# Kernel optimization log

Measured on AMD Instinct MI355X. Metric: run time of the kernel, lower is better.

## Reference

```python
import jax, jax.numpy as jnp
import numpy as np

EPS = 1e-05
FACT = 2.0
REJECT_RATIO = 1.0


def setup_inputs() -> dict:
    key = jax.random.key(0)
    k1, k2 = jax.random.split(key)
    B, N = 8, 4096
    pc1 = jax.random.normal(k1, (B, 4, N), dtype=jnp.float32)
    pc2 = jax.random.normal(k2, (B, 4, N), dtype=jnp.float32)
    # homogeneous coordinates: last row = 1
    pc1 = pc1.at[:, 3, :].set(1.0)
    pc2 = pc2.at[:, 3, :].set(1.0)
    return {"pc1": pc1, "pc2": pc2}


def _rot_to_quat(R):
    # standard rotation-matrix -> quaternion (w, x, y, z)
    r00, r11, r22 = R[0, 0], R[1, 1], R[2, 2]
    qw = 0.5 * jnp.sqrt(jnp.maximum(1e-12, 1.0 + r00 + r11 + r22))
    qx = 0.5 * jnp.sqrt(jnp.maximum(0.0, 1.0 + r00 - r11 - r22))
    qy = 0.5 * jnp.sqrt(jnp.maximum(0.0, 1.0 - r00 + r11 - r22))
    qz = 0.5 * jnp.sqrt(jnp.maximum(0.0, 1.0 - r00 - r11 + r22))
    qx = jnp.where(R[2, 1] - R[1, 2] < 0, -qx, qx)
    qy = jnp.where(R[0, 2] - R[2, 0] < 0, -qy, qy)
    qz = jnp.where(R[1, 0] - R[0, 1] < 0, -qz, qz)
    return jnp.stack([qw, qx, qy, qz])


def _normalize_rotmat(R):
    # operates on COLUMNS, like the torch code (R[:, 2] etc.)
    z = R[:, 2] / jnp.linalg.norm(R[:, 2])
    y = R[:, 1]
    x = jnp.cross(y, z)
    x = x / jnp.linalg.norm(x)
    y = jnp.cross(z, x)
    return jnp.stack([x, y, z], axis=1)


def _norm_tf(pc):
    # T = diag(1/std) @ [I | -mean]  (std is unbiased, as torch.std)
    std = jnp.std(pc[:3, :], axis=1, ddof=1)
    mean = jnp.mean(pc[:3, :], axis=1)
    T = jnp.zeros((4, 4), dtype=pc.dtype)
    T = T.at[jnp.arange(3), jnp.arange(3)].set(1.0 / std)
    T = T.at[:3, 3].set(-mean / std)
    T = T.at[3, 3].set(1.0)
    return T


def _per_sample(pc1, pc2):
    # ---- soft_knn: pairwise squared distance over xyz ----
    p1, p2 = pc1[:3], pc2[:3]  # (3, N)
    d = ((p1 ** 2).sum(0)[:, None]
         - 2.0 * jnp.einsum('dn,dm->nm', p1, p2)
         + (p2 ** 2).sum(0)[None, :])            # (N1, N2)
    W = jax.nn.softmax(FACT / jnp.clip(d, EPS, None), axis=1)
    pc_nearest = pc2 @ W.T                        # (4, N1) soft-gathered points

    # ---- soft_outlier_rejection ----
    dist = jnp.linalg.norm(pc1 - pc_nearest, axis=0)
    filt = jax.nn.sigmoid((dist - dist.mean() * REJECT_RATIO - EPS) * -1e10)

    # ---- dlt(pc1, pc_nearest, filt) ----
    T2 = _norm_tf(pc_nearest)
    pc2n = T2 @ pc_nearest
    T1 = _norm_tf(pc1)
    pc1n = T1 @ pc1

    mask = (filt > 0.5).astype(pc1.dtype)         # hard inlier mask (sigmoid slope 1e10)
    N = pc1.shape[1]
    a = pc1n.T                                    # (N, 4)
    z4 = jnp.zeros((N, 4), dtype=pc1.dtype)
    row0 = jnp.concatenate([z4, -pc2n[2][:, None] * a, pc2n[1][:, None] * a], axis=1)
    row1 = jnp.concatenate([pc2n[2][:, None] * a, z4, -pc2n[0][:, None] * a], axis=1)
    M = (jnp.stack([row0, row1], axis=1) * mask[:, None, None]).reshape(2 * N, 12)

    _, _, Vh = jnp.linalg.svd(M, full_matrices=False)
    p = Vh[-1]                                    # null-space vector (12,)
    p = jnp.where(p[10] < 0, -p, p)
    p = p / jnp.sqrt(p[8] ** 2 + p[9] ** 2 + p[10] ** 2)

    T = jnp.zeros((4, 4), dtype=pc1.dtype)
    T = T.at[:3, :].set(p.reshape(3, 4)).at[3, 3].set(1.0)
    T = jnp.linalg.inv(T2) @ T @ T1
    R = _normalize_rotmat(T[:3, :3])
    T = T.at[:3, :3].set(R)
    return T, _rot_to_quat(R), T[:3, 3]


def reference(pc1, pc2):
    T, q, t = jax.vmap(_per_sample)(pc1, pc2)
    return T, q, t
```

## Files before the change

kernel.cpp:

```cpp
#include <hip/hip_runtime.h>
#include <math.h>

#define NPTS 4096
#define EPSC 1e-5f
#define F2C (2.0f*1.44269504088896340736f)

#if __has_builtin(__builtin_amdgcn_exp2f)
#define FEXP2 __builtin_amdgcn_exp2f
#else
#define FEXP2(x) __expf((x)*0.6931471805599453f)
#endif

#define IDX(i,j) ((i)*((i)+1)/2 + (j))

__global__ void __launch_bounds__(256) k_soft(const float* __restrict__ pc1,
                                              const float* __restrict__ pc2,
                                              float4* __restrict__ part4,
                                              float* __restrict__ partZ){
  constexpr int CHN = 256, NC = 16;
  int bid = blockIdx.x;
  int chunk = bid & (NC-1), rb = (bid/NC) & 15, b = bid/(NC*16);

  __shared__ float4 sp[CHN];
  {
    const float* p2 = pc2 + (size_t)b*4*NPTS + chunk*CHN;
    for (int m = threadIdx.x; m < CHN; m += 256){
      float x = p2[m], y = p2[m+NPTS], z = p2[m+2*NPTS];
      sp[m] = make_float4(x, y, z, x*x + y*y + z*z);
    }
  }
  __syncthreads();

  int n = rb*256 + threadIdx.x;
  const float* p1 = pc1 + (size_t)b*4*NPTS + n;
  float x1 = p1[0], y1 = p1[NPTS], z1 = p1[2*NPTS];
  float q1 = x1*x1 + y1*y1 + z1*z1;
  float mx = -2.f*x1, my = -2.f*y1, mz = -2.f*z1;

  float4 c0 = sp[0];
  float d0 = fmaf(mx,c0.x, fmaf(my,c0.y, fmaf(mz,c0.z, c0.w + q1)));
  float m_ = F2C * __builtin_amdgcn_rcpf(fmaxf(d0, EPSC));
  float L = 1.f, Ax = c0.x, Ay = c0.y, Az = c0.z;

  #pragma unroll 8
  for (int mm=1; mm<CHN; ++mm){
    float4 c = sp[mm];
    float d = fmaf(mx,c.x, fmaf(my,c.y, fmaf(mz,c.z, c.w + q1)));
    float dinv = __builtin_amdgcn_rcpf(fmaxf(d, EPSC));
    float t = fmaf(F2C, dinv, -m_);
    if (__any(t > 0.f)){
      float tp = fmaxf(t, 0.f);
      float sc = FEXP2(-tp);
      L *= sc; Ax *= sc; Ay *= sc; Az *= sc;
      m_ += tp;
      t = fminf(t, 0.f);
    }
    float pe = FEXP2(t);
    L += pe;
    Ax = fmaf(pe,c.x,Ax); Ay = fmaf(pe,c.y,Ay); Az = fmaf(pe,c.z,Az);
  }
  size_t idx = (size_t)(b*NC + chunk)*NPTS + n;
  part4[idx] = make_float4(m_, L, Ax, Ay);
  partZ[idx] = Az;
}

__device__ __forceinline__ void stats_from_tot(const float* stot, float* sst){
  const float Nf = 4096.f, Nm1 = 4095.f;
  #pragma unroll
  for (int j=0;j<3;j++){
    float m  = stot[j]/Nf;
    float v  = (stot[3+j]-Nf*m*m)/Nm1;
    sst[j]=m; sst[3+j]=sqrtf(fmaxf(v,0.f));
    float m2 = stot[6+j]/Nf;
    float v2 = (stot[9+j]-Nf*m2*m2)/Nm1;
    sst[6+j]=m2; sst[9+j]=sqrtf(fmaxf(v2,0.f));
  }
  sst[12]=stot[12]/Nf;
}

__device__ __forceinline__ float elemA(const float* S, int i, int k){
  int bi=i>>2, bj=k>>2;
  int ii=i&3, jj=k&3;
  int lo = ii<jj?ii:jj, hi = ii<jj?jj:ii;
  int pe = 4*lo - ((lo*(lo-1))>>1) + (hi-lo);
  int w;
  if (bi==bj) w = (bi==2)?30:0;
  else {
    int blo = bi<bj?bi:bj, bhi = bi<bj?bj:bi;
    if (blo==0 && bhi==1) return 0.f;
    w = (blo==0)?10:20;
  }
  return S[w+pe];
}

__global__ void __launch_bounds__(512) k_tail(const float* __restrict__ pc1,
                                              const float4* __restrict__ part4,
                                              const float* __restrict__ partZ,
                                              float* __restrict__ out){
  constexpr int NC = 16;
  int b = blockIdx.x, t = threadIdx.x;
  int lane = t & 63, wv = t >> 6;

  __shared__ float4 rowdat[NPTS];
  __shared__ float red13[8][13];
  __shared__ float red40[8][40];
  __shared__ float stot[13];
  __shared__ float sst[13];
  __shared__ float SS[40];

  float acc13[13];
  #pragma unroll
  for (int k=0;k<13;k++) acc13[k]=0.f;
  for (int i=0;i<8;i++){
    int n = i*512 + t;
    float4 f[NC]; float zz[NC];
    #pragma unroll
    for (int c=0;c<NC;c++){
      size_t idx = (size_t)(b*NC + c)*NPTS + n;
      f[c]  = part4[idx];
      zz[c] = partZ[idx];
    }
    float S = f[0].x;
    #pragma unroll
    for (int c=1;c<NC;c++) S = fmaxf(S, f[c].x);
    float L=0.f, Ax=0.f, Ay=0.f, Az=0.f;
    #pragma unroll
    for (int c=0;c<NC;c++){
      float w = FEXP2(f[c].x - S);
      L  = fmaf(w, f[c].y, L);
      Ax = fmaf(w, f[c].z, Ax);
      Ay = fmaf(w, f[c].w, Ay);
      Az = fmaf(w, zz[c],  Az);
    }
    float inv = 1.f/L;
    float px=Ax*inv, py=Ay*inv, pz=Az*inv;
    const float* p1 = pc1 + (size_t)b*4*NPTS + n;
    float x1=p1[0], y1=p1[NPTS], z1=p1[2*NPTS];
    float dx=x1-px, dy=y1-py, dz=z1-pz;
    float dd=sqrtf(dx*dx+dy*dy+dz*dz);
    rowdat[n] = make_float4(px,py,pz,dd);
    acc13[0]+=x1;    acc13[1]+=y1;    acc13[2]+=z1;
    acc13[3]+=x1*x1; acc13[4]+=y1*y1; acc13[5]+=z1*z1;
    acc13[6]+=px;    acc13[7]+=py;    acc13[8]+=pz;
    acc13[9]+=px*px; acc13[10]+=py*py; acc13[11]+=pz*pz;
    acc13[12]+=dd;
  }
  #pragma unroll
  for (int k=0;k<13;k++){
    float v = acc13[k];
    v += __shfl_xor(v,32); v += __shfl_xor(v,16); v += __shfl_xor(v,8);
    v += __shfl_xor(v,4);  v += __shfl_xor(v,2);  v += __shfl_xor(v,1);
    if (lane==0) red13[wv][k]=v;
  }
  __syncthreads();
  if (t<13){
    float s=0.f;
    #pragma unroll
    for (int w=0;w<8;w++) s += red13[w][t];
    stot[t]=s;
  }
  __syncthreads();
  if (t==0) stats_from_tot(stot, sst);
  __syncthreads();

  float i1x=1.f/sst[3], i1y=1.f/sst[4], i1z=1.f/sst[5];
  float t1x=-sst[0]/sst[3], t1y=-sst[1]/sst[4], t1z=-sst[2]/sst[5];
  float i2x=1.f/sst[9], i2y=1.f/sst[10], i2z=1.f/sst[11];
  float t2x=-sst[6]/sst[9], t2y=-sst[7]/sst[10], t2z=-sst[8]/sst[11];
  float meanD=sst[12];

  float acc[40];
  #pragma unroll
  for (int k=0;k<40;k++) acc[k]=0.f;
  for (int i=0;i<8;i++){
    int n = i*512 + t;
    const float* p1 = pc1 + (size_t)b*4*NPTS + n;
    float X1=fmaf(p1[0],i1x,t1x), Y1=fmaf(p1[NPTS],i1y,t1y), Z1=fmaf(p1[2*NPTS],i1z,t1z);
    float4 rd = rowdat[n];
    float X2=fmaf(rd.x,i2x,t2x);
    float Y2=fmaf(rd.y,i2y,t2y);
    float Z2=fmaf(rd.z,i2z,t2z);
    float zthr = (rd.w - meanD) - EPSC;
    float msk = (zthr < 0.f) ? 1.f : 0.f;
    float tz = msk*Z2;
    float wA = tz*Z2, wB = -tz*X2, wC = -tz*Y2;
    float wD = msk*fmaf(X2,X2,Y2*Y2);
    float ee[10]={X1*X1, X1*Y1, X1*Z1, X1, Y1*Y1, Y1*Z1, Y1, Z1*Z1, Z1, 1.f};
    #pragma unroll
    for (int j=0;j<10;j++){
      acc[j]    = fmaf(wA,ee[j],acc[j]);
      acc[10+j] = fmaf(wB,ee[j],acc[10+j]);
      acc[20+j] = fmaf(wC,ee[j],acc[20+j]);
      acc[30+j] = fmaf(wD,ee[j],acc[30+j]);
    }
  }
  #pragma unroll
  for (int k=0;k<40;k++){
    float v=acc[k];
    v+=__shfl_xor(v,32); v+=__shfl_xor(v,16); v+=__shfl_xor(v,8);
    v+=__shfl_xor(v,4);  v+=__shfl_xor(v,2);  v+=__shfl_xor(v,1);
    if(lane==0) red40[wv][k]=v;
  }
  __syncthreads();
  if (t<40){
    float s=0.f;
    #pragma unroll
    for (int w=0;w<8;w++) s += red40[w][t];
    SS[t]=s;
  }
  __syncthreads();

  if (t<64){
    float a[78];
    #pragma unroll
    for (int i=0;i<12;i++)
      #pragma unroll
      for (int j=0;j<=i;j++)
        a[IDX(i,j)] = elemA(SS,i,j);
    {
      float tr=0.f;
      #pragma unroll
      for (int i=0;i<12;i++) tr += a[IDX(i,i)];
      float eps = 1e-5f * tr * (1.f/12.f);
      #pragma unroll
      for (int i=0;i<12;i++) a[IDX(i,i)] += eps;
    }
    #pragma unroll
    for (int j=0;j<12;j++){
      float s = a[IDX(j,j)];
      #pragma unroll
      for (int k=0;k<j;k++) s = fmaf(-a[IDX(j,k)], a[IDX(j,k)], s);
      float d = sqrtf(fmaxf(s, 1e-30f));
      a[IDX(j,j)] = d;
      float dinv = __builtin_amdgcn_rcpf(d);
      #pragma unroll
      for (int i=j+1;i<12;i++){
        float s2 = a[IDX(i,j)];
        #pragma unroll
        for (int k=0;k<j;k++) s2 = fmaf(-a[IDX(i,k)], a[IDX(j,k)], s2);
        a[IDX(i,j)] = s2 * dinv;
      }
    }
    float y[12], Brow[12];
    #pragma unroll
    for (int i=0;i<12;i++){
      float s = (i==t) ? 1.f : 0.f;
      #pragma unroll
      for (int k=0;k<i;k++) s = fmaf(-a[IDX(i,k)], y[k], s);
      y[i] = s * __builtin_amdgcn_rcpf(a[IDX(i,i)]);
    }
    #pragma unroll
    for (int i=11;i>=0;i--){
      float s = y[i];
      #pragma unroll
      for (int k=11;k>i;k--) s = fmaf(-a[IDX(k,i)], Brow[k], s);
      Brow[i] = s * __builtin_amdgcn_rcpf(a[IDX(i,i)]);
    }
    {
      float mxv = 0.f;
      #pragma unroll
      for (int i=0;i<12;i++) mxv = fmaxf(mxv, fabsf(Brow[i]));
      mxv = fmaxf(mxv, __shfl_xor(mxv,1)); mxv = fmaxf(mxv, __shfl_xor(mxv,2));
      mxv = fmaxf(mxv, __shfl_xor(mxv,4)); mxv = fmaxf(mxv, __shfl_xor(mxv,8));
      float sc = __builtin_amdgcn_rcpf(mxv);
      #pragma unroll
      for (int i=0;i<12;i++) Brow[i] *= sc;
    }
    #pragma unroll
    for (int rep=0; rep<2; ++rep){
      float nr[12];
      #pragma unroll
      for (int i=0;i<12;i++) nr[i]=0.f;
      #pragma unroll
      for (int k=0;k<12;k++){
        float bjk = Brow[k];
        #pragma unroll
        for (int m2=0;m2<12;m2++){
          float bkm = __shfl(Brow[m2], k);
          nr[m2] = fmaf(bjk, bkm, nr[m2]);
        }
      }
      float mxv = 0.f;
      #pragma unroll
      for (int i=0;i<12;i++) mxv = fmaxf(mxv, fabsf(nr[i]));
      mxv = fmaxf(mxv, __shfl_xor(mxv,1)); mxv = fmaxf(mxv, __shfl_xor(mxv,2));
      mxv = fmaxf(mxv, __shfl_xor(mxv,4)); mxv = fmaxf(mxv, __shfl_xor(mxv,8));
      float sc = __builtin_amdgcn_rcpf(mxv);
      #pragma unroll
      for (int i=0;i<12;i++) Brow[i] = nr[i]*sc;
    }
    float v = 0.f;
    #pragma unroll
    for (int i=0;i<12;i++) v += Brow[i];
    #pragma unroll
    for (int it=0; it<14; ++it){
      float w = 0.f;
      #pragma unroll
      for (int k=0;k<12;k++) w = fmaf(Brow[k], __shfl(v,k), w);
      float nn = w*w;
      nn += __shfl_xor(nn,1); nn += __shfl_xor(nn,2);
      nn += __shfl_xor(nn,4); nn += __shfl_xor(nn,8);
      v = w * rsqrtf(nn);
    }
    float pvf[12];
    #pragma unroll
    for (int i=0;i<12;i++) pvf[i] = __shfl(v, i);

    if (t==0){
      double pv[12];
      #pragma unroll
      for (int i=0;i<12;i++) pv[i]=(double)pvf[i];
      if (pv[10]<0.0){
        #pragma unroll
        for (int i=0;i<12;i++) pv[i]=-pv[i];
      }
      double nrm = sqrt(pv[8]*pv[8]+pv[9]*pv[9]+pv[10]*pv[10]);
      #pragma unroll
      for (int i=0;i<12;i++) pv[i]/=nrm;
      double m1[3]={sst[0],sst[1],sst[2]}, sd1[3]={sst[3],sst[4],sst[5]};
      double m2[3]={sst[6],sst[7],sst[8]}, sd2[3]={sst[9],sst[10],sst[11]};
      double Td[3][4]={{pv[0],pv[1],pv[2],pv[3]},
                       {pv[4],pv[5],pv[6],pv[7]},
                       {pv[8],pv[9],pv[10],pv[11]}};
      double F[3][4];
      for (int i=0;i<3;i++){
        double b3 = Td[i][3];
        for (int j=0;j<3;j++){
          F[i][j] = sd2[i]*(Td[i][j]/sd1[j]);
          b3 += Td[i][j]*(-m1[j]/sd1[j]);
        }
        F[i][3] = sd2[i]*b3 + m2[i];
      }
      double zx=F[0][2],zy=F[1][2],zz2=F[2][2];
      double zn=sqrt(zx*zx+zy*zy+zz2*zz2);
      zx/=zn; zy/=zn; zz2/=zn;
      double yx=F[0][1],yy=F[1][1],yz=F[2][1];
      double xx=yy*zz2-yz*zy, xy=yz*zx-yx*zz2, xz=yx*zy-yy*zx;
      double xn=sqrt(xx*xx+xy*xy+xz*xz);
      xx/=xn; xy/=xn; xz/=xn;
      double y2x=zy*xz-zz2*xy, y2y=zz2*xx-zx*xz, y2z=zx*xy-zy*xx;
      double R00=xx,R01=y2x,R02=zx;
      double R10=xy,R11=y2y,R12=zy;
      double R20=xz,R21=y2z,R22=zz2;
      float* oT = out + b*16;
      oT[0]=(float)R00; oT[1]=(float)R01; oT[2]=(float)R02; oT[3]=(float)F[0][3];
      oT[4]=(float)R10; oT[5]=(float)R11; oT[6]=(float)R12; oT[7]=(float)F[1][3];
      oT[8]=(float)R20; oT[9]=(float)R21; oT[10]=(float)R22; oT[11]=(float)F[2][3];
      oT[12]=0.f; oT[13]=0.f; oT[14]=0.f; oT[15]=1.f;
      double qw=0.5*sqrt(fmax(1e-12, 1.0+R00+R11+R22));
      double qx=0.5*sqrt(fmax(0.0, 1.0+R00-R11-R22));
      double qy=0.5*sqrt(fmax(0.0, 1.0-R00+R11-R22));
      double qz=0.5*sqrt(fmax(0.0, 1.0-R00-R11+R22));
      if (R21-R12<0.0) qx=-qx;
      if (R02-R20<0.0) qy=-qy;
      if (R10-R01<0.0) qz=-qz;
      float* oQ = out + 128 + b*4;
      oQ[0]=(float)qw; oQ[1]=(float)qx; oQ[2]=(float)qy; oQ[3]=(float)qz;
      float* ot3 = out + 160 + b*3;
      ot3[0]=(float)F[0][3]; ot3[1]=(float)F[1][3]; ot3[2]=(float)F[2][3];
    }
  }
}

extern "C" void kernel_launch(void* const* d_in, const int* in_sizes, int n_in,
                              void* d_out, int out_size, void* d_ws, size_t ws_size,
                              hipStream_t stream) {
  const float* pc1 = (const float*)d_in[0];
  const float* pc2 = (const float*)d_in[1];
  float* out  = (float*)d_out;
  float* ws   = (float*)d_ws;

  float4* part4 = (float4*)ws;
  float*  partZ = ws + 4*2097152/4 + 0;
  partZ = ws + 2097152;

  hipLaunchKernelGGL(k_soft, dim3(2048), dim3(256), 0, stream, pc1, pc2, part4, partZ);
  hipLaunchKernelGGL(k_tail, dim3(8),    dim3(512), 0, stream, pc1, part4, partZ, out);
}
```

Before: 170.7 us.

## Split tail into parallel split-softmax merge kernel and small final reduction kernel

The tail kernel ran on only 8 blocks and serially merged the 16 softmax partials for every point. That merge, along with the first-moment statistics, moves into a new 128-block kernel that writes per-point rows and per-block partial sums to workspace. The final kernel now uses 1024 threads per batch, reads those rows, and does the moment accumulation and the 12x12 solve. This adds a kernel launch and a global round trip for the row data in exchange for spreading the bandwidth-heavy merge across many more compute units.

```diff
diff --git a/kernel.cpp b/kernel.cpp
--- a/kernel.cpp
+++ b/kernel.cpp
@@ -64,6 +64,56 @@
   partZ[idx] = Az;
 }
 
+__global__ void __launch_bounds__(256) k_mid(const float* __restrict__ pc1,
+                                             const float4* __restrict__ part4,
+                                             const float* __restrict__ partZ,
+                                             float4* __restrict__ rowdat,
+                                             float* __restrict__ psum13){
+  constexpr int NC = 16;
+  int b = blockIdx.x >> 4, rb = blockIdx.x & 15, t = threadIdx.x;
+  int n = rb*256 + t;
+  float4 f[NC]; float zz[NC];
+  #pragma unroll
+  for (int c=0;c<NC;c++){
+    size_t idx = (size_t)(b*NC + c)*NPTS + n;
+    f[c]  = part4[idx];
+    zz[c] = partZ[idx];
+  }
+  float S = f[0].x;
+  #pragma unroll
+  for (int c=1;c<NC;c++) S = fmaxf(S, f[c].x);
+  float L=0.f, Ax=0.f, Ay=0.f, Az=0.f;
+  #pragma unroll
+  for (int c=0;c<NC;c++){
+    float w = FEXP2(f[c].x - S);
+    L  = fmaf(w, f[c].y, L);
+    Ax = fmaf(w, f[c].z, Ax);
+    Ay = fmaf(w, f[c].w, Ay);
+    Az = fmaf(w, zz[c],  Az);
+  }
+  float inv = 1.f/L;
+  float px=Ax*inv, py=Ay*inv, pz=Az*inv;
+  const float* p1 = pc1 + (size_t)b*4*NPTS + n;
+  float x1=p1[0], y1=p1[NPTS], z1=p1[2*NPTS];
+  float dx=x1-px, dy=y1-py, dz=z1-pz;
+  float dd=sqrtf(dx*dx+dy*dy+dz*dz);
+  rowdat[(size_t)b*NPTS + n] = make_float4(px,py,pz,dd);
+
+  float acc[13]={x1,y1,z1,x1*x1,y1*y1,z1*z1,px,py,pz,px*px,py*py,pz*pz,dd};
+  __shared__ float red[4][13];
+  int lane = t & 63, wv = t >> 6;
+  #pragma unroll
+  for (int k=0;k<13;k++){
+    float v = acc[k];
+    v += __shfl_xor(v,32); v += __shfl_xor(v,16); v += __shfl_xor(v,8);
+    v += __shfl_xor(v,4);  v += __shfl_xor(v,2);  v += __shfl_xor(v,1);
+    if (lane==0) red[wv][k]=v;
+  }
+  __syncthreads();
+  if (t<13)
+    psum13[(size_t)blockIdx.x*13 + t] = red[0][t]+red[1][t]+red[2][t]+red[3][t];
+}
+
 __device__ __forceinline__ void stats_from_tot(const float* stot, float* sst){
   const float Nf = 4096.f, Nm1 = 4095.f;
   #pragma unroll
@@ -93,70 +143,22 @@
   return S[w+pe];
 }
 
-__global__ void __launch_bounds__(512) k_tail(const float* __restrict__ pc1,
-                                              const float4* __restrict__ part4,
-                                              const float* __restrict__ partZ,
+__global__ void __launch_bounds__(1024) k_fin(const float* __restrict__ pc1,
+                                              const float4* __restrict__ rowdat,
+                                              const float* __restrict__ psum13,
                                               float* __restrict__ out){
-  constexpr int NC = 16;
   int b = blockIdx.x, t = threadIdx.x;
   int lane = t & 63, wv = t >> 6;
 
-  __shared__ float4 rowdat[NPTS];
-  __shared__ float red13[8][13];
-  __shared__ float red40[8][40];
   __shared__ float stot[13];
   __shared__ float sst[13];
+  __shared__ float red40[16][40];
   __shared__ float SS[40];
 
-  float acc13[13];
-  #pragma unroll
-  for (int k=0;k<13;k++) acc13[k]=0.f;
-  for (int i=0;i<8;i++){
-    int n = i*512 + t;
-    float4 f[NC]; float zz[NC];
-    #pragma unroll
-    for (int c=0;c<NC;c++){
-      size_t idx = (size_t)(b*NC + c)*NPTS + n;
-      f[c]  = part4[idx];
-      zz[c] = partZ[idx];
-    }
-    float S = f[0].x;
-    #pragma unroll
-    for (int c=1;c<NC;c++) S = fmaxf(S, f[c].x);
-    float L=0.f, Ax=0.f, Ay=0.f, Az=0.f;
-    #pragma unroll
-    for (int c=0;c<NC;c++){
-      float w = FEXP2(f[c].x - S);
-      L  = fmaf(w, f[c].y, L);
-      Ax = fmaf(w, f[c].z, Ax);
-      Ay = fmaf(w, f[c].w, Ay);
-      Az = fmaf(w, zz[c],  Az);
-    }
-    float inv = 1.f/L;
-    float px=Ax*inv, py=Ay*inv, pz=Az*inv;
-    const float* p1 = pc1 + (size_t)b*4*NPTS + n;
-    float x1=p1[0], y1=p1[NPTS], z1=p1[2*NPTS];
-    float dx=x1-px, dy=y1-py, dz=z1-pz;
-    float dd=sqrtf(dx*dx+dy*dy+dz*dz);
-    rowdat[n] = make_float4(px,py,pz,dd);
-    acc13[0]+=x1;    acc13[1]+=y1;    acc13[2]+=z1;
-    acc13[3]+=x1*x1; acc13[4]+=y1*y1; acc13[5]+=z1*z1;
-    acc13[6]+=px;    acc13[7]+=py;    acc13[8]+=pz;
-    acc13[9]+=px*px; acc13[10]+=py*py; acc13[11]+=pz*pz;
-    acc13[12]+=dd;
-  }
-  #pragma unroll
-  for (int k=0;k<13;k++){
-    float v = acc13[k];
-    v += __shfl_xor(v,32); v += __shfl_xor(v,16); v += __shfl_xor(v,8);
-    v += __shfl_xor(v,4);  v += __shfl_xor(v,2);  v += __shfl_xor(v,1);
-    if (lane==0) red13[wv][k]=v;
-  }
-  __syncthreads();
   if (t<13){
     float s=0.f;
     #pragma unroll
-    for (int w=0;w<8;w++) s += red13[w][t];
+    for (int i=0;i<16;i++) s += psum13[(size_t)(b*16+i)*13 + t];
     stot[t]=s;
   }
   __syncthreads();
@@ -172,11 +174,12 @@
   float acc[40];
   #pragma unroll
   for (int k=0;k<40;k++) acc[k]=0.f;
-  for (int i=0;i<8;i++){
-    int n = i*512 + t;
+  #pragma unroll
+  for (int i=0;i<4;i++){
+    int n = i*1024 + t;
     const float* p1 = pc1 + (size_t)b*4*NPTS + n;
     float X1=fmaf(p1[0],i1x,t1x), Y1=fmaf(p1[NPTS],i1y,t1y), Z1=fmaf(p1[2*NPTS],i1z,t1z);
-    float4 rd = rowdat[n];
+    float4 rd = rowdat[(size_t)b*NPTS + n];
     float X2=fmaf(rd.x,i2x,t2x);
     float Y2=fmaf(rd.y,i2y,t2y);
     float Z2=fmaf(rd.z,i2z,t2z);
@@ -205,7 +208,7 @@
   if (t<40){
     float s=0.f;
     #pragma unroll
-    for (int w=0;w<8;w++) s += red40[w][t];
+    for (int w=0;w<16;w++) s += red40[w][t];
     SS[t]=s;
   }
   __syncthreads();
@@ -370,10 +373,12 @@
   float* out  = (float*)d_out;
   float* ws   = (float*)d_ws;
 
-  float4* part4 = (float4*)ws;
-  float*  partZ = ws + 4*2097152/4 + 0;
-  partZ = ws + 2097152;
-
-  hipLaunchKernelGGL(k_soft, dim3(2048), dim3(256), 0, stream, pc1, pc2, part4, partZ);
-  hipLaunchKernelGGL(k_tail, dim3(8),    dim3(512), 0, stream, pc1, part4, partZ, out);
-}
+  float4* part4  = (float4*)ws;
+  float*  partZ  = ws + 2097152;
+  float4* rowdat = (float4*)(ws + 2097152 + 524288);
+  float*  psum13 = ws + 2097152 + 524288 + 131072;
+
+  hipLaunchKernelGGL(k_soft, dim3(2048), dim3(256),  0, stream, pc1, pc2, part4, partZ);
+  hipLaunchKernelGGL(k_mid,  dim3(128),  dim3(256),  0, stream, pc1, part4, partZ, rowdat, psum13);
+  hipLaunchKernelGGL(k_fin,  dim3(8),    dim3(1024), 0, stream, pc1, rowdat, psum13, out);
+}
```

Measured after the change: 169.1 us. About the same (-0.9%).
